# Optimization experiments

Hardware: AMD Instinct MI355X
Metric: run time of the kernel (lower is better)

The kernel has to match this reference:

```python
import jax, jax.numpy as jnp
import numpy as np

B, S, E, H = 2, 2048, 2048, 16
HD = E // H  # head dim (value_factor = 1, so key dim == value dim)
EPS = 1e-5


def setup_inputs() -> dict:
    key = jax.random.key(0)
    ks = jax.random.split(key, 12)
    std = 0.02

    def lin(k, din, dout):
        kw, kb = jax.random.split(k)
        W = jax.random.normal(kw, (din, dout), jnp.float32) * std  # stored [in,out]
        b = jnp.zeros((dout,), jnp.float32)
        return W, b

    x = jax.random.normal(ks[0], (B, S, E), jnp.float32)
    Wq, bq = lin(ks[1], E, E)
    Wk, bk = lin(ks[2], E, E)
    Wv, bv = lin(ks[3], E, E)
    Wg, bg = lin(ks[4], E, E)
    Wo, bo = lin(ks[5], E, E)
    gn_w = jnp.ones((E,), jnp.float32)
    gn_b = jnp.zeros((E,), jnp.float32)
    decay = jnp.log(1.0 - 2.0 ** (-5.0 - jnp.arange(H, dtype=jnp.float32)))
    return dict(x=x, Wq=Wq, bq=bq, Wk=Wk, bk=bk, Wv=Wv, bv=bv,
                Wg=Wg, bg=bg, Wo=Wo, bo=bo, gn_w=gn_w, gn_b=gn_b, decay=decay)


def _retention(x, Wq, bq, Wk, bk, Wv, bv, Wg, bg, Wo, bo, gn_w, gn_b, decay):
    b, s, e = x.shape
    h = decay.shape[0]
    hd = e // h
    scaling = hd ** -0.5

    def heads(t):  # [b, s, e] -> [b, h, s, hd]
        return t.reshape(b, s, h, hd).transpose(0, 2, 1, 3)

    q = heads((x @ Wq + bq) * scaling)
    k = heads(x @ Wk + bk)
    v = heads(x @ Wv + bv)

    # causal decay mask D[h,i,j] = gamma_h^(i-j) for i>=j, else 0
    idx = jnp.arange(s)
    diff = idx[:, None] - idx[None, :]               # [s, s]
    causal = diff >= 0
    diff_c = jnp.where(causal, diff, 0).astype(jnp.float32)
    D = jnp.where(causal[None], jnp.exp(decay[:, None, None] * diff_c[None]), 0.0)  # [h,s,s]

    ret = jnp.einsum('bhid,bhjd->bhij', q, k) * D[None]      # [b,h,s,s]
    # per-row abs-sum normalization (detached scale, clamped at 1)
    scale = jnp.clip(jnp.abs(jax.lax.stop_gradient(ret).sum(-1, keepdims=True)), 1.0, None)
    ret = ret / scale
    attn = jnp.einsum('bhij,bhjd->bhid', ret, v)             # [b,h,s,hd]
    attn = attn.transpose(0, 2, 1, 3).reshape(b, s, e)       # [b,s,e]

    # GroupNorm(num_groups=h, num_channels=e) applied per token
    g = attn.reshape(b, s, h, hd)
    mu = g.mean(-1, keepdims=True)
    var = g.var(-1, keepdims=True)
    g = (g - mu) / jnp.sqrt(var + EPS)
    g = g.reshape(b, s, e) * gn_w + gn_b

    gate = jax.nn.silu(x @ Wg + bg)
    return (gate * g) @ Wo + bo


def reference(x, Wq, bq, Wk, bk, Wv, bv, Wg, bg, Wo, bo, gn_w, gn_b, decay):
    return _retention(x, Wq, bq, Wk, bk, Wv, bv, Wg, bg, Wo, bo, gn_w, gn_b, decay)
```

## Files before the change

kernel.cpp:

```cpp
#include <hip/hip_runtime.h>
#include <math.h>

#define Bn 2
#define Sn 2048
#define En 2048
#define Hn 16
#define HDn 128

typedef __attribute__((ext_vector_type(8))) short short8;
typedef __attribute__((ext_vector_type(4))) float f32x4;
typedef unsigned short u16;
typedef unsigned int u32;

__device__ __forceinline__ float bf2f(u16 x){
  union { u32 u; float f; } v; v.u = ((u32)x) << 16; return v.f;
}
__device__ __forceinline__ u16 f2bf(float f){
  union { float f; u32 u; } v; v.f = f;
  u32 r = v.u + 0x7fff + ((v.u >> 16) & 1);
  return (u16)(r >> 16);
}
__device__ __forceinline__ void gload16(const u16* g, u16* l){
  __builtin_amdgcn_global_load_lds((const __attribute__((address_space(1))) void*)g,
                                   (__attribute__((address_space(3))) void*)l, 16, 0, 0);
}

__global__ void detect_dtype(const u16* __restrict__ x, int* __restrict__ flag){
  int lane = threadIdx.x;
  int cnt = 0;
  #pragma unroll
  for (int i = 0; i < 4; i++){
    u16 u = x[lane*4 + i];
    int e = (u >> 7) & 0xFF;
    cnt += (e < 96 || e > 159) ? 1 : 0;
  }
  cnt += __shfl_xor(cnt, 1);  cnt += __shfl_xor(cnt, 2);  cnt += __shfl_xor(cnt, 4);
  cnt += __shfl_xor(cnt, 8);  cnt += __shfl_xor(cnt, 16); cnt += __shfl_xor(cnt, 32);
  if (lane == 0) flag[0] = (cnt > 32) ? 1 : 0;
}

__global__ __launch_bounds__(256) void convert_x(const void* __restrict__ xin, u16* __restrict__ xb,
                                                 const int* __restrict__ flag){
  long i8 = ((long)blockIdx.x*256 + threadIdx.x)*8;
  if (flag[0]){
    const float* xf = (const float*)xin;
    float4 a = *(const float4*)(xf + i8);
    float4 b = *(const float4*)(xf + i8 + 4);
    u16 t[8] = {f2bf(a.x),f2bf(a.y),f2bf(a.z),f2bf(a.w),f2bf(b.x),f2bf(b.y),f2bf(b.z),f2bf(b.w)};
    *(uint4*)(xb + i8) = *(uint4*)t;
  } else {
    *(uint4*)(xb + i8) = *(const uint4*)((const u16*)xin + i8);
  }
}

__device__ __forceinline__ void transpose_body(const void* __restrict__ in, u16* __restrict__ out,
                                               int blk, int f){
  __shared__ __align__(16) u16 t[64][72];
  int bx = blk & 31;
  int by = blk >> 5;
  int tid = threadIdx.x;
  #pragma unroll
  for (int c = tid; c < 512; c += 256){
    int r = c >> 3, col = (c & 7) << 3;
    long base = (long)((by<<6)+r)*2048 + (bx<<6) + col;
    u16 tmp[8];
    if (f){
      const float* pf = (const float*)in + base;
      float4 a = *(const float4*)pf;
      float4 b = *(const float4*)(pf + 4);
      tmp[0]=f2bf(a.x); tmp[1]=f2bf(a.y); tmp[2]=f2bf(a.z); tmp[3]=f2bf(a.w);
      tmp[4]=f2bf(b.x); tmp[5]=f2bf(b.y); tmp[6]=f2bf(b.z); tmp[7]=f2bf(b.w);
    } else {
      *(uint4*)tmp = *(const uint4*)((const u16*)in + base);
    }
    *(uint4*)&t[r][col] = *(uint4*)tmp;
  }
  __syncthreads();
  #pragma unroll
  for (int c = tid; c < 512; c += 256){
    int r = c >> 3, col = (c & 7) << 3;
    u16 tmp[8];
    #pragma unroll
    for (int i = 0; i < 8; i++) tmp[i] = t[col + i][r];
    *(uint4*)(out + (long)((bx<<6)+r)*2048 + (by<<6) + col) = *(uint4*)tmp;
  }
}

__global__ __launch_bounds__(256) void transpose2048(const void* __restrict__ in, u16* __restrict__ out,
                                                     const int* __restrict__ flag){
  transpose_body(in, out, blockIdx.x, flag[0]);
}

__global__ __launch_bounds__(256) void transpose4(const void* __restrict__ in0, const void* __restrict__ in1,
                const void* __restrict__ in2, const void* __restrict__ in3,
                u16* __restrict__ out, const int* __restrict__ flag){
  int which = blockIdx.x >> 10;
  const void* in = (which==0)?in0:(which==1)?in1:(which==2)?in2:in3;
  u16* o = out + (size_t)which*((size_t)2048*2048);
  transpose_body(in, o, blockIdx.x & 1023, flag[0]);
}

__global__ __launch_bounds__(256) void gemm_bt(const u16* __restrict__ A, const u16* __restrict__ Bt,
                const void* __restrict__ bias, void* __restrict__ C,
                int Mdim, int Ndim, int Kdim, int mode, float scale,
                const int* __restrict__ flag, int outfp){
  __shared__ __align__(16) u16 As[128*32];
  __shared__ __align__(16) u16 Bs[128*32];
  int blk = blockIdx.x;
  int st = blk & 7, lid = blk >> 3;
  int m0 = ((st >> 1)*8 + (lid & 7)) << 7;
  int n0 = ((st & 1)*8 + (lid >> 3)) << 7;
  int tid = threadIdx.x;
  int w = tid >> 6, lane = tid & 63, l16 = lane & 15, quad = lane >> 4;
  int wm = w & 1, wn = w >> 1;
  int f = flag[0];
  int sr = lane >> 2;
  int sc = (lane & 3) << 3;
  const u16* gA = A  + (long)(m0 + (w<<5) + sr)*Kdim + sc;
  const u16* gB = Bt + (long)(n0 + (w<<5) + sr)*Kdim + sc;
  u16* lA0 = As + (w<<5)*32;  u16* lA1 = lA0 + 512;
  u16* lB0 = Bs + (w<<5)*32;  u16* lB1 = lB0 + 512;
  const long rowskip = (long)16*Kdim;

  f32x4 acc[4][4];
  #pragma unroll
  for (int i = 0; i < 4; i++)
    #pragma unroll
    for (int j = 0; j < 4; j++) acc[i][j] = (f32x4){0.f,0.f,0.f,0.f};

  for (int k0 = 0; k0 < Kdim; k0 += 32){
    __syncthreads();
    gload16(gA + k0,           lA0);
    gload16(gA + k0 + rowskip, lA1);
    gload16(gB + k0,           lB0);
    gload16(gB + k0 + rowskip, lB1);
    __syncthreads();
    short8 af[4], bfr[4];
    #pragma unroll
    for (int mf = 0; mf < 4; mf++) af[mf]  = *(const short8*)&As[(wm*64 + mf*16 + l16)*32 + quad*8];
    #pragma unroll
    for (int nf = 0; nf < 4; nf++) bfr[nf] = *(const short8*)&Bs[(wn*64 + nf*16 + l16)*32 + quad*8];
    #pragma unroll
    for (int mf = 0; mf < 4; mf++)
      #pragma unroll
      for (int nf = 0; nf < 4; nf++)
        acc[mf][nf] = __builtin_amdgcn_mfma_f32_16x16x32_bf16(af[mf], bfr[nf], acc[mf][nf], 0, 0, 0);
  }
  #pragma unroll
  for (int nf = 0; nf < 4; nf++){
    int col = n0 + wn*64 + nf*16 + l16;
    float bv = f ? ((const float*)bias)[col] : bf2f(((const u16*)bias)[col]);
    #pragma unroll
    for (int mf = 0; mf < 4; mf++){
      #pragma unroll
      for (int r = 0; r < 4; r++){
        int row = m0 + wm*64 + mf*16 + quad*4 + r;
        float v = acc[mf][nf][r] + bv;
        if (mode == 1) v *= scale;
        else if (mode == 2) v = v / (1.0f + __expf(-v));
        long idx = (long)row*Ndim + col;
        if (outfp && f) ((float*)C)[idx] = v;
        else            ((u16*)C)[idx] = f2bf(v);
      }
    }
  }
}

__global__ __launch_bounds__(512, 2) void gemm4_8ph(const u16* __restrict__ A, const u16* __restrict__ Wt4,
                const void* __restrict__ bq_, const void* __restrict__ bk_,
                const void* __restrict__ bv_, const void* __restrict__ bg_,
                u16* __restrict__ qo, u16* __restrict__ ko, u16* __restrict__ vo, u16* __restrict__ go,
                const int* __restrict__ flag, float qscale){
  __shared__ __align__(16) u16 LDS[65536];
  const size_t WE = (size_t)2048*2048;
  int blk = blockIdx.x;
  int xcd = blk & 7, lid = blk >> 3;
  int m0 = (((xcd << 1) | (lid & 1))) << 8;
  int n0 = ((lid >> 1) & 7) << 8;
  int wsel = (lid >> 4) & 3;
  const u16* Bt = Wt4 + WE*(size_t)wsel;
  const void* bias = (wsel==0) ? bq_ : (wsel==1) ? bk_ : (wsel==2) ? bv_ : bg_;
  u16* Cout = (wsel==0) ? qo : (wsel==1) ? ko : (wsel==2) ? vo : go;
  int tid = threadIdx.x;
  int w = tid >> 6, lane = tid & 63, l16 = lane & 15, quad = lane >> 4;
  int wm = w >> 2, wn = w & 3;
  int f = flag[0];

  int srowA = tid >> 3;
  int srowB = ((w >> 2) << 6) | ((w & 3) << 3) | ((tid >> 3) & 7);
  int sg = ((tid & 7) ^ ((tid >> 3) & 7)) << 3;
  const u16* gA = A  + (long)(m0 + srowA)*2048 + sg;
  const u16* gB = Bt + (long)(n0 + srowB)*2048 + sg;
  u16* ldsA = LDS;
  u16* ldsB = LDS + 32768;
  const int wofsA = w << 9;
  const int wofsB = ((w >> 2) << 12) | ((w & 3) << 9);

  int g0 = quad ^ (l16 & 7);
  const int abase = (wm*128 + l16) * 64;
  const int bbase = (wn*64  + l16) * 64;

  f32x4 acc[8][4];
  #pragma unroll
  for (int i = 0; i < 8; i++)
    #pragma unroll
    for (int j = 0; j < 4; j++) acc[i][j] = (f32x4){0.f,0.f,0.f,0.f};
  short8 a[4][2], b0[2][2], b1[2][2];

#define STG_A(buf, tt, h) do{ \
  gload16(gA + (long)((h)*64)*2048       + (tt)*64, ldsA + (buf)*16384 + (h)*4096 + wofsA); \
  gload16(gA + (long)(128 + (h)*64)*2048 + (tt)*64, ldsA + (buf)*16384 + 8192 + (h)*4096 + wofsA); \
}while(0)
#define STG_B(buf, tt, h) do{ \
  gload16(gB + (long)((h)*32)*2048       + (tt)*64, ldsB + (buf)*16384 + (h)*2048 + wofsB); \
  gload16(gB + (long)(128 + (h)*32)*2048 + (tt)*64, ldsB + (buf)*16384 + 8192 + (h)*2048 + wofsB); \
}while(0)
#define LDA_Q(buf, qm) do{ \
  _Pragma("unroll") for (int m_ = 0; m_ < 4; m_++) \
  _Pragma("unroll") for (int ks_ = 0; ks_ < 2; ks_++) \
    a[m_][ks_] = *(const short8*)(ldsA + (buf)*16384 + abase + ((qm)*64 + m_*16)*64 + ((g0 ^ (ks_<<2))<<3)); \
}while(0)
#define LDB_Q(arr, buf, qn) do{ \
  _Pragma("unroll") for (int n_ = 0; n_ < 2; n_++) \
  _Pragma("unroll") for (int ks_ = 0; ks_ < 2; ks_++) \
    arr[n_][ks_] = *(const short8*)(ldsB + (buf)*16384 + bbase + (((qn)*2 + n_)*16)*64 + ((g0 ^ (ks_<<2))<<3)); \
}while(0)
#define MFMAQ(qm, qn, arr) do{ \
  _Pragma("unroll") for (int ks_ = 0; ks_ < 2; ks_++) \
  _Pragma("unroll") for (int m_ = 0; m_ < 4; m_++) \
  _Pragma("unroll") for (int n_ = 0; n_ < 2; n_++) \
    acc[(qm)*4 + m_][(qn)*2 + n_] = __builtin_amdgcn_mfma_f32_16x16x32_bf16( \
        a[m_][ks_], arr[n_][ks_], acc[(qm)*4 + m_][(qn)*2 + n_], 0, 0, 0); \
}while(0)
#define PH_TAIL(qm, qn, arr) do{ \
  asm volatile("" ::: "memory"); \
  __builtin_amdgcn_s_barrier(); \
  asm volatile("s_waitcnt lgkmcnt(0)" ::: "memory"); \
  __builtin_amdgcn_sched_barrier(0); \
  __builtin_amdgcn_s_setprio(1); \
  MFMAQ(qm, qn, arr); \
  __builtin_amdgcn_s_setprio(0); \
  __builtin_amdgcn_sched_barrier(0); \
  asm volatile("" ::: "memory"); \
  __builtin_amdgcn_s_barrier(); \
}while(0)

  STG_A(0, 0, 0);
  STG_B(0, 0, 1);
  STG_A(0, 0, 1);
  STG_B(0, 0, 0);
  STG_A(1, 1, 0);
  STG_B(1, 1, 1);
  STG_A(1, 1, 1);
  asm volatile("s_waitcnt vmcnt(6)" ::: "memory");
  __builtin_amdgcn_s_barrier();

  #pragma unroll 1
  for (int i = 0; i < 16; i++){
    const int t = i << 1;
    const bool full = (i < 15);
    LDA_Q(0, 0); LDB_Q(b0, 0, 0);
    STG_B(1, t + 1, 0);
    asm volatile("s_waitcnt lgkmcnt(8)" ::: "memory");
    PH_TAIL(0, 0, b0);
    LDB_Q(b1, 0, 1);
    if (full) STG_A(0, t + 2, 0);
    PH_TAIL(0, 1, b1);
    LDA_Q(0, 1);
    if (full) STG_B(0, t + 2, 1);
    PH_TAIL(1, 1, b1);
    if (full){
      STG_A(0, t + 2, 1);
      asm volatile("s_waitcnt vmcnt(6)" ::: "memory");
    } else {
      asm volatile("s_waitcnt vmcnt(0)" ::: "memory");
    }
    PH_TAIL(1, 0, b0);
    LDA_Q(1, 0); LDB_Q(b0, 1, 0);
    if (full) STG_B(0, t + 2, 0);
    asm volatile("s_waitcnt lgkmcnt(8)" ::: "memory");
    PH_TAIL(0, 0, b0);
    LDB_Q(b1, 1, 1);
    if (full) STG_A(1, t + 3, 0);
    PH_TAIL(0, 1, b1);
    LDA_Q(1, 1);
    if (full) STG_B(1, t + 3, 1);
    PH_TAIL(1, 1, b1);
    if (full){
      STG_A(1, t + 3, 1);
      asm volatile("s_waitcnt vmcnt(6)" ::: "memory");
    }
    PH_TAIL(1, 0, b0);
  }

#undef STG_A
#undef STG_B
#undef LDA_Q
#undef LDB_Q
#undef MFMAQ
#undef PH_TAIL

  __syncthreads();
  #pragma unroll
  for (int nf = 0; nf < 4; nf++){
    int colL = wn*64 + nf*16 + l16;
    float bv = f ? ((const float*)bias)[n0 + colL] : bf2f(((const u16*)bias)[n0 + colL]);
    #pragma unroll
    for (int mf = 0; mf < 8; mf++){
      #pragma unroll
      for (int r = 0; r < 4; r++){
        int rowL = wm*128 + mf*16 + quad*4 + r;
        float v = acc[mf][nf][r] + bv;
        if (wsel == 0) v *= qscale;
        else if (wsel == 3) v = v / (1.0f + __expf(-v));
        LDS[rowL*256 + colL] = f2bf(v);
      }
    }
  }
  __syncthreads();
  #pragma unroll
  for (int it2 = 0; it2 < 16; it2++){
    int idx = it2*4096 + tid*8;
    int rowL = idx >> 8, colL = idx & 255;
    *(uint4*)(Cout + (long)(m0 + rowL)*2048 + n0 + colL) = *(const uint4*)(LDS + idx);
  }
}

__global__ __launch_bounds__(256) void retention(const u16* __restrict__ q, const u16* __restrict__ k,
     const u16* __restrict__ v, const u16* __restrict__ gate, const void* __restrict__ gnw,
     const void* __restrict__ gnb, const void* __restrict__ decay, u16* __restrict__ gated,
     const int* __restrict__ flag){
  __shared__ __align__(16) u16 Ks[64][136];
  __shared__ __align__(16) u16 Vt[128][72];
  __shared__ __align__(16) u16 Ss[4][16][72];
  int bh = blockIdx.x & 31;
  int it = 31 - (blockIdx.x >> 5);
  int b = bh >> 4, h = bh & 15;
  int f = flag[0];
  float dec = f ? ((const float*)decay)[h] : bf2f(((const u16*)decay)[h]);
  int tid = threadIdx.x, w = tid >> 6, lane = tid & 63, l16 = lane & 15, quad = lane >> 4;

  float gw8[8], gb8[8];
  #pragma unroll
  for (int nf = 0; nf < 8; nf++){
    int ch = h*HDn + nf*16 + l16;
    gw8[nf] = f ? ((const float*)gnw)[ch] : bf2f(((const u16*)gnw)[ch]);
    gb8[nf] = f ? ((const float*)gnb)[ch] : bf2f(((const u16*)gnb)[ch]);
  }
  float ei4[4], ejl[4];
  #pragma unroll
  for (int r = 0; r < 4; r++) ei4[r] = __expf(dec * (float)(w*16 + quad*4 + r));
  #pragma unroll
  for (int nf = 0; nf < 4; nf++) ejl[nf] = __expf(-dec * (float)(nf*16 + l16));

  int i0 = it << 6;
  short8 qf[4];
  {
    int qrow = i0 + w*16 + l16;
    const u16* qbase = q + (long)(b*Sn + qrow)*En + h*HDn;
    #pragma unroll
    for (int kf = 0; kf < 4; kf++){
      uint4 t = *(const uint4*)(qbase + kf*32 + quad*8);
      qf[kf] = *(short8*)&t;
    }
  }
  f32x4 oacc[8];
  #pragma unroll
  for (int i = 0; i < 8; i++) oacc[i] = (f32x4){0.f,0.f,0.f,0.f};
  float rs[4] = {0.f,0.f,0.f,0.f};

  int njt = it + 1;
  uint4 kreg[4], vreg[4];
  #pragma unroll
  for (int t = 0; t < 4; t++){
    int c = tid + t*256;
    int jr = c >> 4, dc = (c & 15) << 3;
    kreg[t] = *(const uint4*)(k + (long)(b*Sn + jr)*En + h*HDn + dc);
    int jr2 = c & 63, dc2 = (c >> 6) << 3;
    vreg[t] = *(const uint4*)(v + (long)(b*Sn + jr2)*En + h*HDn + dc2);
  }

  for (int jt = 0; jt < njt; jt++){
    int j0 = jt << 6;
    float etile = __expf(dec * (float)(i0 - j0));
    float em[4];
    #pragma unroll
    for (int r = 0; r < 4; r++) em[r] = etile * ei4[r];
    __syncthreads();
    #pragma unroll
    for (int t = 0; t < 4; t++){
      int c = tid + t*256;
      int jr = c >> 4, dc = (c & 15) << 3;
      *(uint4*)&Ks[jr][dc] = kreg[t];
      int jr2 = c & 63, dc2 = (c >> 6) << 3;
      u16 tmp[8]; *(uint4*)tmp = vreg[t];
      #pragma unroll
      for (int i = 0; i < 8; i++) Vt[dc2 + i][jr2] = tmp[i];
    }
    __syncthreads();
    if (jt + 1 < njt){
      int jn = j0 + 64;
      #pragma unroll
      for (int t = 0; t < 4; t++){
        int c = tid + t*256;
        int jr = c >> 4, dc = (c & 15) << 3;
        kreg[t] = *(const uint4*)(k + (long)(b*Sn + jn + jr)*En + h*HDn + dc);
        int jr2 = c & 63, dc2 = (c >> 6) << 3;
        vreg[t] = *(const uint4*)(v + (long)(b*Sn + jn + jr2)*En + h*HDn + dc2);
      }
    }
    #pragma unroll
    for (int nf = 0; nf < 4; nf++){
      f32x4 s = (f32x4){0.f,0.f,0.f,0.f};
      #pragma unroll
      for (int kf = 0; kf < 4; kf++){
        short8 kfr = *(const short8*)&Ks[nf*16 + l16][kf*32 + quad*8];
        s = __builtin_amdgcn_mfma_f32_16x16x32_bf16(qf[kf], kfr, s, 0, 0, 0);
      }
      int j = j0 + nf*16 + l16;
      #pragma unroll
      for (int r = 0; r < 4; r++){
        int i = i0 + w*16 + quad*4 + r;
        float p = s[r] * em[r] * ejl[nf];
        p = (i >= j) ? p : 0.0f;
        rs[r] += p;
        Ss[w][quad*4 + r][nf*16 + l16] = f2bf(p);
      }
    }
    asm volatile("" ::: "memory");
    __builtin_amdgcn_s_waitcnt(0xC07F);
    asm volatile("" ::: "memory");
    #pragma unroll
    for (int kf = 0; kf < 2; kf++){
      short8 pa = *(const short8*)&Ss[w][l16][kf*32 + quad*8];
      #pragma unroll
      for (int nf = 0; nf < 8; nf++){
        short8 vf = *(const short8*)&Vt[nf*16 + l16][kf*32 + quad*8];
        oacc[nf] = __builtin_amdgcn_mfma_f32_16x16x32_bf16(pa, vf, oacc[nf], 0, 0, 0);
      }
    }
  }
  #pragma unroll
  for (int r = 0; r < 4; r++){
    float x = rs[r];
    x += __shfl_xor(x, 1); x += __shfl_xor(x, 2); x += __shfl_xor(x, 4); x += __shfl_xor(x, 8);
    float sc = 1.0f / fmaxf(fabsf(x), 1.0f);
    #pragma unroll
    for (int nf = 0; nf < 8; nf++) oacc[nf][r] *= sc;
  }
  float mu[4], rstd[4];
  #pragma unroll
  for (int r = 0; r < 4; r++){
    float s1 = 0.f, s2 = 0.f;
    #pragma unroll
    for (int nf = 0; nf < 8; nf++){ float xv = oacc[nf][r]; s1 += xv; s2 += xv*xv; }
    s1 += __shfl_xor(s1, 1); s1 += __shfl_xor(s1, 2); s1 += __shfl_xor(s1, 4); s1 += __shfl_xor(s1, 8);
    s2 += __shfl_xor(s2, 1); s2 += __shfl_xor(s2, 2); s2 += __shfl_xor(s2, 4); s2 += __shfl_xor(s2, 8);
    float m = s1 * (1.0f/128.0f);
    float var = s2 * (1.0f/128.0f) - m*m;
    mu[r] = m; rstd[r] = rsqrtf(fmaxf(var, 0.0f) + 1e-5f);
  }
  #pragma unroll
  for (int nf = 0; nf < 8; nf++){
    int ch = h*HDn + nf*16 + l16;
    #pragma unroll
    for (int r = 0; r < 4; r++){
      int row = i0 + w*16 + quad*4 + r;
      long ga = (long)(b*Sn + row)*En + ch;
      float g = (oacc[nf][r] - mu[r]) * rstd[r] * gw8[nf] + gb8[nf];
      float gt = bf2f(gate[ga]);
      gated[ga] = f2bf(gt * g);
    }
  }
}

extern "C" void kernel_launch(void* const* d_in, const int* in_sizes, int n_in,
                              void* d_out, int out_size, void* d_ws, size_t ws_size,
                              hipStream_t stream){
  const void* x   = d_in[0];
  const void* Wq  = d_in[1];
  const void* bq  = d_in[2];
  const void* Wk  = d_in[3];
  const void* bk  = d_in[4];
  const void* Wv  = d_in[5];
  const void* bv  = d_in[6];
  const void* Wg  = d_in[7];
  const void* bg  = d_in[8];
  const void* Wo  = d_in[9];
  const void* bo  = d_in[10];
  const void* gnw = d_in[11];
  const void* gnb = d_in[12];
  const void* dec = d_in[13];

  u16* base = (u16*)d_ws;
  const size_t WE = (size_t)2048*2048;
  const size_t AE = (size_t)4096*2048;
  const float qscale = 0.08838834764831845f;
  u16* gatebuf = (u16*)d_out;

  const size_t fused_bytes = (AE*4 + WE*4)*2 + 64;

  if (ws_size >= fused_bytes){
    u16* xb  = base;
    u16* Wt4 = xb + AE;
    u16* qb  = Wt4 + 4*WE;
    u16* kb  = qb + AE;
    u16* vb  = kb + AE;
    int* flag = (int*)(vb + AE);
    u16* gtd = qb;

    detect_dtype<<<1, 64, 0, stream>>>((const u16*)x, flag);
    convert_x<<<4096, 256, 0, stream>>>(x, xb, flag);
    transpose4<<<4096, 256, 0, stream>>>(Wq, Wk, Wv, Wg, Wt4, flag);

    gemm4_8ph<<<512, 512, 0, stream>>>(xb, Wt4, bq, bk, bv, bg, qb, kb, vb, gatebuf, flag, qscale);

    retention<<<1024, 256, 0, stream>>>(qb, kb, vb, gatebuf, gnw, gnb, dec, gtd, flag);

    transpose2048<<<1024, 256, 0, stream>>>(Wo, Wt4, flag);
    gemm_bt<<<512, 256, 0, stream>>>(gtd, Wt4, bo, d_out, 4096, 2048, 2048, 0, 1.0f, flag, 1);
  } else {
    u16* xb = base;
    u16* Wt = xb + AE;
    u16* qb = Wt + WE;
    u16* kb = qb + AE;
    u16* vb = kb + AE;
    int* flag = (int*)(vb + AE);
    u16* gtd = qb;

    detect_dtype<<<1, 64, 0, stream>>>((const u16*)x, flag);
    convert_x<<<4096, 256, 0, stream>>>(x, xb, flag);

    transpose2048<<<1024, 256, 0, stream>>>(Wq, Wt, flag);
    gemm_bt<<<512, 256, 0, stream>>>(xb, Wt, bq, qb, 4096, 2048, 2048, 1, qscale, flag, 0);
    transpose2048<<<1024, 256, 0, stream>>>(Wk, Wt, flag);
    gemm_bt<<<512, 256, 0, stream>>>(xb, Wt, bk, kb, 4096, 2048, 2048, 0, 1.0f, flag, 0);
    transpose2048<<<1024, 256, 0, stream>>>(Wv, Wt, flag);
    gemm_bt<<<512, 256, 0, stream>>>(xb, Wt, bv, vb, 4096, 2048, 2048, 0, 1.0f, flag, 0);
    transpose2048<<<1024, 256, 0, stream>>>(Wg, Wt, flag);
    gemm_bt<<<512, 256, 0, stream>>>(xb, Wt, bg, gatebuf, 4096, 2048, 2048, 2, 1.0f, flag, 0);

    retention<<<1024, 256, 0, stream>>>(qb, kb, vb, gatebuf, gnw, gnb, dec, gtd, flag);

    transpose2048<<<1024, 256, 0, stream>>>(Wo, Wt, flag);
    gemm_bt<<<512, 256, 0, stream>>>(gtd, Wt, bo, d_out, 4096, 2048, 2048, 0, 1.0f, flag, 1);
  }
}
```

Before: 477.9 us.

## Prefetch B fragments inside MFMA phase and merge Wo transpose into batch

The 8-phase QKVG GEMM now issues the next iteration's first B-fragment LDS load inside the last MFMA phase, after the MFMAs and before the barrier, instead of waiting on it at the head of the next phase. This is meant to hide LDS read latency behind compute and drop the explicit lgkmcnt waits. Separately, when the workspace is large enough, Wo is transposed together with the other four weights in a single transpose5 launch, removing one kernel launch before the output GEMM. The cost is one more weight-sized workspace buffer and a more delicate LDS load ordering.

```diff
diff --git a/kernel.cpp b/kernel.cpp
--- a/kernel.cpp
+++ b/kernel.cpp
@@ -96,6 +96,15 @@
                 u16* __restrict__ out, const int* __restrict__ flag){
   int which = blockIdx.x >> 10;
   const void* in = (which==0)?in0:(which==1)?in1:(which==2)?in2:in3;
+  u16* o = out + (size_t)which*((size_t)2048*2048);
+  transpose_body(in, o, blockIdx.x & 1023, flag[0]);
+}
+
+__global__ __launch_bounds__(256) void transpose5(const void* __restrict__ in0, const void* __restrict__ in1,
+                const void* __restrict__ in2, const void* __restrict__ in3, const void* __restrict__ in4,
+                u16* __restrict__ out, const int* __restrict__ flag){
+  int which = blockIdx.x >> 10;
+  const void* in = (which==0)?in0:(which==1)?in1:(which==2)?in2:(which==3)?in3:in4;
   u16* o = out + (size_t)which*((size_t)2048*2048);
   transpose_body(in, o, blockIdx.x & 1023, flag[0]);
 }
@@ -215,32 +224,33 @@
   gload16(gB + (long)((h)*32)*2048       + (tt)*64, ldsB + (buf)*16384 + (h)*2048 + wofsB); \
   gload16(gB + (long)(128 + (h)*32)*2048 + (tt)*64, ldsB + (buf)*16384 + 8192 + (h)*2048 + wofsB); \
 }while(0)
-#define LDA_Q(buf, qm) do{ \
+#define LDA_Q(dst, buf, qm) do{ \
   _Pragma("unroll") for (int m_ = 0; m_ < 4; m_++) \
   _Pragma("unroll") for (int ks_ = 0; ks_ < 2; ks_++) \
-    a[m_][ks_] = *(const short8*)(ldsA + (buf)*16384 + abase + ((qm)*64 + m_*16)*64 + ((g0 ^ (ks_<<2))<<3)); \
+    dst[m_][ks_] = *(const short8*)(ldsA + (buf)*16384 + abase + ((qm)*64 + m_*16)*64 + ((g0 ^ (ks_<<2))<<3)); \
 }while(0)
-#define LDB_Q(arr, buf, qn) do{ \
+#define LDB_Q(dst, buf, qn) do{ \
   _Pragma("unroll") for (int n_ = 0; n_ < 2; n_++) \
   _Pragma("unroll") for (int ks_ = 0; ks_ < 2; ks_++) \
-    arr[n_][ks_] = *(const short8*)(ldsB + (buf)*16384 + bbase + (((qn)*2 + n_)*16)*64 + ((g0 ^ (ks_<<2))<<3)); \
+    dst[n_][ks_] = *(const short8*)(ldsB + (buf)*16384 + bbase + (((qn)*2 + n_)*16)*64 + ((g0 ^ (ks_<<2))<<3)); \
 }while(0)
-#define MFMAQ(qm, qn, arr) do{ \
+#define MFMAQ(qm, qn, barr) do{ \
   _Pragma("unroll") for (int ks_ = 0; ks_ < 2; ks_++) \
   _Pragma("unroll") for (int m_ = 0; m_ < 4; m_++) \
   _Pragma("unroll") for (int n_ = 0; n_ < 2; n_++) \
     acc[(qm)*4 + m_][(qn)*2 + n_] = __builtin_amdgcn_mfma_f32_16x16x32_bf16( \
-        a[m_][ks_], arr[n_][ks_], acc[(qm)*4 + m_][(qn)*2 + n_], 0, 0, 0); \
+        a[m_][ks_], barr[n_][ks_], acc[(qm)*4 + m_][(qn)*2 + n_], 0, 0, 0); \
 }while(0)
-#define PH_TAIL(qm, qn, arr) do{ \
+#define PH_TAIL(qm, qn, barr, ...) do{ \
   asm volatile("" ::: "memory"); \
   __builtin_amdgcn_s_barrier(); \
   asm volatile("s_waitcnt lgkmcnt(0)" ::: "memory"); \
   __builtin_amdgcn_sched_barrier(0); \
   __builtin_amdgcn_s_setprio(1); \
-  MFMAQ(qm, qn, arr); \
+  MFMAQ(qm, qn, barr); \
   __builtin_amdgcn_s_setprio(0); \
   __builtin_amdgcn_sched_barrier(0); \
+  __VA_ARGS__; \
   asm volatile("" ::: "memory"); \
   __builtin_amdgcn_s_barrier(); \
 }while(0)
@@ -254,19 +264,19 @@
   STG_A(1, 1, 1);
   asm volatile("s_waitcnt vmcnt(6)" ::: "memory");
   __builtin_amdgcn_s_barrier();
+  LDB_Q(b0, 0, 0);
 
   #pragma unroll 1
   for (int i = 0; i < 16; i++){
     const int t = i << 1;
     const bool full = (i < 15);
-    LDA_Q(0, 0); LDB_Q(b0, 0, 0);
+    LDA_Q(a, 0, 0);
     STG_B(1, t + 1, 0);
-    asm volatile("s_waitcnt lgkmcnt(8)" ::: "memory");
     PH_TAIL(0, 0, b0);
     LDB_Q(b1, 0, 1);
     if (full) STG_A(0, t + 2, 0);
     PH_TAIL(0, 1, b1);
-    LDA_Q(0, 1);
+    LDA_Q(a, 0, 1);
     if (full) STG_B(0, t + 2, 1);
     PH_TAIL(1, 1, b1);
     if (full){
@@ -275,22 +285,23 @@
     } else {
       asm volatile("s_waitcnt vmcnt(0)" ::: "memory");
     }
-    PH_TAIL(1, 0, b0);
-    LDA_Q(1, 0); LDB_Q(b0, 1, 0);
+    PH_TAIL(1, 0, b0, LDB_Q(b0, 1, 0));
+    LDA_Q(a, 1, 0);
     if (full) STG_B(0, t + 2, 0);
-    asm volatile("s_waitcnt lgkmcnt(8)" ::: "memory");
     PH_TAIL(0, 0, b0);
     LDB_Q(b1, 1, 1);
     if (full) STG_A(1, t + 3, 0);
     PH_TAIL(0, 1, b1);
-    LDA_Q(1, 1);
+    LDA_Q(a, 1, 1);
     if (full) STG_B(1, t + 3, 1);
     PH_TAIL(1, 1, b1);
     if (full){
       STG_A(1, t + 3, 1);
       asm volatile("s_waitcnt vmcnt(6)" ::: "memory");
-    }
-    PH_TAIL(1, 0, b0);
+      PH_TAIL(1, 0, b0, LDB_Q(b0, 0, 0));
+    } else {
+      PH_TAIL(1, 0, b0);
+    }
   }
 
 #undef STG_A
@@ -498,12 +509,14 @@
   const float qscale = 0.08838834764831845f;
   u16* gatebuf = (u16*)d_out;
 
-  const size_t fused_bytes = (AE*4 + WE*4)*2 + 64;
+  const size_t fused_bytes  = (AE*4 + WE*4)*2 + 64;
+  const size_t fused5_bytes = (AE*4 + WE*5)*2 + 64;
 
   if (ws_size >= fused_bytes){
+    int five = (ws_size >= fused5_bytes) ? 1 : 0;
     u16* xb  = base;
-    u16* Wt4 = xb + AE;
-    u16* qb  = Wt4 + 4*WE;
+    u16* Wt  = xb + AE;
+    u16* qb  = Wt + (five ? 5 : 4)*WE;
     u16* kb  = qb + AE;
     u16* vb  = kb + AE;
     int* flag = (int*)(vb + AE);
@@ -511,14 +524,19 @@
 
     detect_dtype<<<1, 64, 0, stream>>>((const u16*)x, flag);
     convert_x<<<4096, 256, 0, stream>>>(x, xb, flag);
-    transpose4<<<4096, 256, 0, stream>>>(Wq, Wk, Wv, Wg, Wt4, flag);
-
-    gemm4_8ph<<<512, 512, 0, stream>>>(xb, Wt4, bq, bk, bv, bg, qb, kb, vb, gatebuf, flag, qscale);
+    if (five) transpose5<<<5120, 256, 0, stream>>>(Wq, Wk, Wv, Wg, Wo, Wt, flag);
+    else      transpose4<<<4096, 256, 0, stream>>>(Wq, Wk, Wv, Wg, Wt, flag);
+
+    gemm4_8ph<<<512, 512, 0, stream>>>(xb, Wt, bq, bk, bv, bg, qb, kb, vb, gatebuf, flag, qscale);
 
     retention<<<1024, 256, 0, stream>>>(qb, kb, vb, gatebuf, gnw, gnb, dec, gtd, flag);
 
-    transpose2048<<<1024, 256, 0, stream>>>(Wo, Wt4, flag);
-    gemm_bt<<<512, 256, 0, stream>>>(gtd, Wt4, bo, d_out, 4096, 2048, 2048, 0, 1.0f, flag, 1);
+    if (five){
+      gemm_bt<<<512, 256, 0, stream>>>(gtd, Wt + 4*WE, bo, d_out, 4096, 2048, 2048, 0, 1.0f, flag, 1);
+    } else {
+      transpose2048<<<1024, 256, 0, stream>>>(Wo, Wt, flag);
+      gemm_bt<<<512, 256, 0, stream>>>(gtd, Wt, bo, d_out, 4096, 2048, 2048, 0, 1.0f, flag, 1);
+    }
   } else {
     u16* xb = base;
     u16* Wt = xb + AE;
```

After: 471.9 us. About the same (-1.3%).
